# Optimization experiments

Measured on AMD Instinct MI355X. Metric: run time of the kernel, lower is better.

Reference implementation:

```python
import jax, jax.numpy as jnp
import numpy as np

L, D, H, DK, FF, R, N, B = 8, 256, 8, 32, 1024, 37, 1024, 1
EPS = 1e-6


def setup_inputs() -> dict:
    key = jax.random.key(0)
    ks = jax.random.split(key, 16)
    def w(i, shape, s=0.05):
        return jax.random.normal(ks[i], shape, jnp.float32) * s
    return {
        "x": jax.random.normal(ks[0], (B, N, D), jnp.float32),
        "relations": jax.random.randint(ks[1], (N, N), 0, R),
        "Wq": w(2, (L, D, D)), "bq": jnp.zeros((L, D), jnp.float32),
        "Wk": w(3, (L, D, D)), "bk": jnp.zeros((L, D), jnp.float32),
        "Wv": w(4, (L, D, D)), "bv": jnp.zeros((L, D), jnp.float32),
        "Wo": w(5, (L, D, D)), "bo": jnp.zeros((L, D), jnp.float32),
        "rel_k_emb": w(6, (L, R, DK)), "rel_v_emb": w(7, (L, R, DK)),
        "W1": w(8, (L, D, FF)), "b1": jnp.zeros((L, FF), jnp.float32),
        "W2": w(9, (L, FF, D)), "b2": jnp.zeros((L, D), jnp.float32),
        "ln1_g": jnp.ones((L, D), jnp.float32), "ln1_b": jnp.zeros((L, D), jnp.float32),
        "ln2_g": jnp.ones((L, D), jnp.float32), "ln2_b": jnp.zeros((L, D), jnp.float32),
        "lnf_g": jnp.ones((D,), jnp.float32), "lnf_b": jnp.zeros((D,), jnp.float32),
    }


def _layernorm(h, g, b):
    # Annotated-Transformer LayerNorm: g*(x-mu)/(std+eps)+b with unbiased std
    mu = h.mean(-1, keepdims=True)
    sd = jnp.sqrt(h.var(-1, keepdims=True, ddof=1))
    return g * (h - mu) / (sd + EPS) + b


def reference(x, relations, Wq, bq, Wk, bk, Wv, bv, Wo, bo,
              rel_k_emb, rel_v_emb, W1, b1, W2, b2,
              ln1_g, ln1_b, ln2_g, ln2_b, lnf_g, lnf_b):
    Bb, n, d = x.shape
    scale = 1.0 / jnp.sqrt(jnp.float32(DK))
    for l in range(L):
        # --- relation-aware self-attention sublayer (pre-norm residual) ---
        xn = _layernorm(x, ln1_g[l], ln1_b[l])
        q = (xn @ Wq[l] + bq[l]).reshape(Bb, n, H, DK).transpose(0, 2, 1, 3)
        k = (xn @ Wk[l] + bk[l]).reshape(Bb, n, H, DK).transpose(0, 2, 1, 3)
        v = (xn @ Wv[l] + bv[l]).reshape(Bb, n, H, DK).transpose(0, 2, 1, 3)
        rk = rel_k_emb[l][relations]  # [n, n, DK] irregular gather
        rv = rel_v_emb[l][relations]  # [n, n, DK]
        scores = (jnp.einsum('bhid,bhjd->bhij', q, k)
                  + jnp.einsum('bhid,ijd->bhij', q, rk)) * scale
        p = jax.nn.softmax(scores, axis=-1)
        o = (jnp.einsum('bhij,bhjd->bhid', p, v)
             + jnp.einsum('bhij,ijd->bhid', p, rv))
        o = o.transpose(0, 2, 1, 3).reshape(Bb, n, d) @ Wo[l] + bo[l]
        x = x + o
        # --- position-wise FFN sublayer (pre-norm residual) ---
        xn = _layernorm(x, ln2_g[l], ln2_b[l])
        x = x + (jax.nn.relu(xn @ W1[l] + b1[l]) @ W2[l] + b2[l])
    return _layernorm(x, lnf_g, lnf_b)
```

## Files before the change

kernel.cpp:

```cpp
#include <hip/hip_runtime.h>
#include <stdint.h>

#define L_ 8
#define D_ 256
#define H_ 8
#define DK_ 32
#define FF_ 1024
#define R_ 37
#define N_ 1024
#define AIB 32

#define SCL (0.17677669529663689f * 1.4426950408889634f)

typedef float f4v __attribute__((ext_vector_type(4)));
typedef short b8v __attribute__((ext_vector_type(8)));
typedef uint  u2v __attribute__((ext_vector_type(2)));

__device__ __forceinline__ ushort f2b(float f){
  union { float f; uint32_t u; } x; x.f = f;
  return (ushort)((x.u + 0x7FFFu + ((x.u >> 16) & 1u)) >> 16);
}
__device__ __forceinline__ float b2f(ushort u){
  union { uint32_t u; float f; } x; x.u = ((uint32_t)u) << 16;
  return x.f;
}
__device__ __forceinline__ uint pk2b(float lo, float hi){
  return (((uint)f2b(hi)) << 16) | (uint)f2b(lo);
}
__device__ __forceinline__ float ex2(float x){ return __builtin_amdgcn_exp2f(x); }

__device__ __forceinline__ void lds_fadd(float* p, float v){
  asm volatile("ds_add_f32 %0, %1" :: "v"((uint)(uintptr_t)p), "v"(v) : "memory");
}

__global__ __launch_bounds__(256)
void wcast_kernel(const float* __restrict__ src, ushort* __restrict__ dst, int K, int Nc){
  __shared__ float t[32][33];
  int l = blockIdx.z;
  long base = (long)l * K * Nc;
  int n0 = blockIdx.x * 32, k0 = blockIdx.y * 32;
  int tx = threadIdx.x, ty = threadIdx.y;
  #pragma unroll
  for (int r = 0; r < 32; r += 8)
    t[ty + r][tx] = src[base + (long)(k0 + ty + r) * Nc + n0 + tx];
  __syncthreads();
  #pragma unroll
  for (int r = 0; r < 32; r += 8)
    dst[base + (long)(n0 + ty + r) * K + k0 + tx] = f2b(t[tx][ty + r]);
}

__global__ __launch_bounds__(256)
void rel8_kernel(const int* __restrict__ rel, uint* __restrict__ rel8){
  long idx = (long)blockIdx.x * 256 + threadIdx.x;
  int4 v = ((const int4*)rel)[idx];
  rel8[idx] = (uint)(v.x & 255) | ((uint)(v.y & 255) << 8)
            | ((uint)(v.z & 255) << 16) | ((uint)(v.w & 255) << 24);
}

template<int OUTB>
__global__ __launch_bounds__(64)
void ln_kernel(const float* __restrict__ x, const float* __restrict__ g, const float* __restrict__ b,
               ushort* __restrict__ ob, float* __restrict__ of){
  int row = blockIdx.x, lane = threadIdx.x;
  float4 v = ((const float4*)(x + (long)row * D_))[lane];
  float s = v.x + v.y + v.z + v.w;
  float s2 = v.x*v.x + v.y*v.y + v.z*v.z + v.w*v.w;
  #pragma unroll
  for (int o = 32; o; o >>= 1){ s += __shfl_xor(s, o); s2 += __shfl_xor(s2, o); }
  float mu = s * (1.f / D_);
  float var = (s2 - D_ * mu * mu) * (1.f / (D_ - 1));
  var = fmaxf(var, 0.f);
  float inv = 1.f / (sqrtf(var) + 1e-6f);
  float4 gv = ((const float4*)g)[lane];
  float4 bv = ((const float4*)b)[lane];
  float o0 = gv.x * (v.x - mu) * inv + bv.x;
  float o1 = gv.y * (v.y - mu) * inv + bv.y;
  float o2 = gv.z * (v.z - mu) * inv + bv.z;
  float o3 = gv.w * (v.w - mu) * inv + bv.w;
  if (OUTB){
    ushort4 u; u.x = f2b(o0); u.y = f2b(o1); u.z = f2b(o2); u.w = f2b(o3);
    ((ushort4*)ob)[(long)row * 64 + lane] = u;
  } else {
    float4 o; o.x = o0; o.y = o1; o.z = o2; o.w = o3;
    ((float4*)of)[(long)row * 64 + lane] = o;
  }
}

template<int QKV, int RELU, int RESID, int OUTF, int OUTB>
__global__ __launch_bounds__(256)
void gemm_kernel(const ushort* __restrict__ A,
                 const ushort* __restrict__ W0, const ushort* __restrict__ W1p, const ushort* __restrict__ W2p,
                 const float* __restrict__ B0, const float* __restrict__ B1p, const float* __restrict__ B2p,
                 float* __restrict__ resid, float* __restrict__ outF, ushort* __restrict__ outB,
                 ushort* __restrict__ outB2,
                 int M, int Nc, int K){
  __shared__ ushort Al[64 * 48];
  __shared__ ushort Bl[64 * 48];
  int tid = threadIdx.x;
  int lane = tid & 63, w = tid >> 6;
  int wm = w >> 1, wn = w & 1;
  int bn0 = blockIdx.x * 64, bm0 = blockIdx.y * 64;
  const ushort* WT; const float* bias; int wn0;
  if (QKV){
    int which = bn0 >> 8;
    WT = which == 0 ? W0 : (which == 1 ? W1p : W2p);
    bias = which == 0 ? B0 : (which == 1 ? B1p : B2p);
    wn0 = bn0 & 255;
  } else { WT = W0; bias = B0; wn0 = bn0; }

  int r4 = tid >> 2, c8 = (tid & 3) * 8;
  const ushort* ag = A + (long)(bm0 + r4) * K + c8;
  const ushort* bg = WT + (long)(wn0 + r4) * K + c8;

  f4v acc[2][2];
  #pragma unroll
  for (int i = 0; i < 2; ++i)
    #pragma unroll
    for (int j = 0; j < 2; ++j)
      acc[i][j] = (f4v){0.f, 0.f, 0.f, 0.f};

  int l16 = lane & 15, lg = lane >> 4;
  int arow0 = (wm * 32 + l16) * 48 + lg * 8;
  int brow0 = (wn * 32 + l16) * 48 + lg * 8;

  for (int k0 = 0; k0 < K; k0 += 32){
    b8v a8 = *(const b8v*)(ag + k0);
    b8v b8 = *(const b8v*)(bg + k0);
    __syncthreads();
    *(b8v*)&Al[r4 * 48 + c8] = a8;
    *(b8v*)&Bl[r4 * 48 + c8] = b8;
    __syncthreads();
    b8v a0 = *(const b8v*)&Al[arow0];
    b8v a1 = *(const b8v*)&Al[arow0 + 16 * 48];
    b8v b0 = *(const b8v*)&Bl[brow0];
    b8v b1 = *(const b8v*)&Bl[brow0 + 16 * 48];
    acc[0][0] = __builtin_amdgcn_mfma_f32_16x16x32_bf16(a0, b0, acc[0][0], 0, 0, 0);
    acc[0][1] = __builtin_amdgcn_mfma_f32_16x16x32_bf16(a0, b1, acc[0][1], 0, 0, 0);
    acc[1][0] = __builtin_amdgcn_mfma_f32_16x16x32_bf16(a1, b0, acc[1][0], 0, 0, 0);
    acc[1][1] = __builtin_amdgcn_mfma_f32_16x16x32_bf16(a1, b1, acc[1][1], 0, 0, 0);
  }
  #pragma unroll
  for (int fi = 0; fi < 2; ++fi)
    #pragma unroll
    for (int fj = 0; fj < 2; ++fj){
      int row0 = bm0 + wm * 32 + fi * 16 + lg * 4;
      int col = bn0 + wn * 32 + fj * 16 + l16;
      float vv[4];
      #pragma unroll
      for (int j = 0; j < 4; ++j) vv[j] = acc[fi][fj][j] + bias[QKV ? (col & 255) : col];
      if (QKV){
        int which = col >> 8, hh = (col >> 5) & 7, dk = col & 31;
        if (which == 2){
          ushort4 pk; pk.x = f2b(vv[0]); pk.y = f2b(vv[1]); pk.z = f2b(vv[2]); pk.w = f2b(vv[3]);
          *(ushort4*)(outB2 + (long)hh * 32768 + (long)dk * 1024 + row0) = pk;
        } else {
          #pragma unroll
          for (int j = 0; j < 4; ++j)
            outB[(long)which * 262144 + (long)hh * 32768 + (long)(row0 + j) * 32 + dk] = f2b(vv[j]);
        }
      } else {
        #pragma unroll
        for (int j = 0; j < 4; ++j){
          float v = vv[j];
          if (RELU) v = fmaxf(v, 0.f);
          long idx = (long)(row0 + j) * Nc + col;
          if (RESID) v += resid[idx];
          if (OUTF) outF[idx] = v;
          if (OUTB) outB[idx] = f2b(v);
        }
      }
    }
}

__global__ __launch_bounds__(512)
void attn_kernel(const ushort* __restrict__ qb, const ushort* __restrict__ kb,
                 const ushort* __restrict__ vbt, const float* __restrict__ rke,
                 const float* __restrict__ rve,
                 const unsigned char* __restrict__ rel8, ushort* __restrict__ ob){
  __shared__ float q_l[AIB * 32];
  __shared__ float qr_l[AIB * 40];
  __shared__ float prb[4 * AIB * 40];
  __shared__ uint  p_l[8 * 16 * 20];
  __shared__ float part_l[4 * AIB * 34];
  __shared__ float wf_l[4 * AIB];
  __shared__ float lrow_l[AIB];

  int tid = threadIdx.x, lane = tid & 63, w = tid >> 6;
  int l16 = lane & 15, g = lane >> 4;
  int ib0 = blockIdx.x * AIB, h = blockIdx.y;
  int js = w >> 1, ig = w & 1;
  int ir = ig * 16 + l16;

  if (tid < 256){
    int row = tid >> 3, d4 = (tid & 7) * 4;
    ushort4 u = *(const ushort4*)(qb + (long)((h << 10) + ib0 + row) * 32 + d4);
    q_l[row * 32 + d4 + 0] = b2f(u.x);
    q_l[row * 32 + d4 + 1] = b2f(u.y);
    q_l[row * 32 + d4 + 2] = b2f(u.z);
    q_l[row * 32 + d4 + 3] = b2f(u.w);
  }
  for (int idx = tid; idx < 4 * AIB * 40; idx += 512) prb[idx] = 0.f;
  __syncthreads();

  for (int slot = tid; slot < AIB * 40; slot += 512){
    int row = slot / 40, r = slot - row * 40;
    if (r < R_){
      const float* qh = &q_l[row * 32];
      const float* e = rke + r * 32;
      float acc = 0.f;
      #pragma unroll
      for (int d = 0; d < 32; ++d) acc += qh[d] * e[d];
      qr_l[slot] = acc * SCL;
    }
  }
  __syncthreads();

  b8v qf = *(const b8v*)(qb + (long)((h << 10) + ib0 + ir) * 32 + g * 8);

  f4v oacc0 = (f4v){0.f,0.f,0.f,0.f}, oacc1 = (f4v){0.f,0.f,0.f,0.f};
  float m = -3.0e38f, lsum = 0.f;
  const float* qrr = &qr_l[ir * 40];
  float* prr = &prb[(js * AIB + ir) * 40];
  const unsigned char* relrow = rel8 + (long)(ib0 + ir) * N_ + js * 256;
  const ushort* kbh = kb + (long)(h << 10) * 32;
  const ushort* vth = vbt + (long)h * 32 * 1024;
  uint* pw = &p_l[w * 320 + l16 * 20];

  #pragma unroll
  for (int jt = 0; jt < 8; ++jt){
    int j0 = js * 256 + jt * 32;
    b8v kf0 = *(const b8v*)(kbh + (long)(j0 + l16) * 32 + g * 8);
    b8v kf1 = *(const b8v*)(kbh + (long)(j0 + 16 + l16) * 32 + g * 8);
    b8v vt0 = *(const b8v*)(vth + (long)l16 * 1024 + j0 + g * 8);
    b8v vt1 = *(const b8v*)(vth + (long)(16 + l16) * 1024 + j0 + g * 8);
    uint rr0 = *(const uint*)(relrow + jt * 32 + g * 4);
    uint rr1 = *(const uint*)(relrow + jt * 32 + 16 + g * 4);

    f4v z = (f4v){0.f,0.f,0.f,0.f};
    f4v s0 = __builtin_amdgcn_mfma_f32_16x16x32_bf16(kf0, qf, z, 0, 0, 0);
    f4v s1 = __builtin_amdgcn_mfma_f32_16x16x32_bf16(kf1, qf, z, 0, 0, 0);

    int rix[8];
    float sv[8];
    #pragma unroll
    for (int e = 0; e < 4; ++e){
      rix[e]     = (rr0 >> (8 * e)) & 255;
      rix[e + 4] = (rr1 >> (8 * e)) & 255;
      sv[e]     = s0[e] * SCL + qrr[rix[e]];
      sv[e + 4] = s1[e] * SCL + qrr[rix[e + 4]];
    }
    float tmax = sv[0];
    #pragma unroll
    for (int e = 1; e < 8; ++e) tmax = fmaxf(tmax, sv[e]);
    tmax = fmaxf(tmax, __shfl_xor(tmax, 16));
    tmax = fmaxf(tmax, __shfl_xor(tmax, 32));

    if (tmax - m > 12.f){
      float f = ex2(m - tmax);
      oacc0 *= f; oacc1 *= f; lsum *= f;
      #pragma unroll
      for (int b2 = 0; b2 < 10; ++b2){
        int bi = g * 10 + b2;
        if (bi < R_) prr[bi] *= f;
      }
      m = tmax;
    }
    float p[8], ps = 0.f;
    #pragma unroll
    for (int e = 0; e < 8; ++e){ p[e] = ex2(sv[e] - m); ps += p[e]; }
    ps += __shfl_xor(ps, 16);
    ps += __shfl_xor(ps, 32);
    lsum += ps;
    #pragma unroll
    for (int e = 0; e < 8; ++e) lds_fadd(&prr[rix[e]], p[e]);

    uint pk0 = pk2b(p[0], p[1]), pk1 = pk2b(p[2], p[3]);
    uint pk2 = pk2b(p[4], p[5]), pk3 = pk2b(p[6], p[7]);
    *(u2v*)&pw[g * 2]     = (u2v){pk0, pk1};
    *(u2v*)&pw[8 + g * 2] = (u2v){pk2, pk3};
    b8v pf = *(const b8v*)&pw[g * 4];
    oacc0 = __builtin_amdgcn_mfma_f32_16x16x32_bf16(vt0, pf, oacc0, 0, 0, 0);
    oacc1 = __builtin_amdgcn_mfma_f32_16x16x32_bf16(vt1, pf, oacc1, 0, 0, 0);
  }

  {
    float* pp = &part_l[(js * AIB + ir) * 34];
    #pragma unroll
    for (int e = 0; e < 4; ++e){
      pp[g * 4 + e] = oacc0[e];
      pp[16 + g * 4 + e] = oacc1[e];
    }
    if (g == 0){ pp[32] = m; pp[33] = lsum; }
  }
  __syncthreads();

  if (tid < AIB){
    int row = tid;
    float ms[4], ls[4];
    float mstar = -3.0e38f;
    #pragma unroll
    for (int s = 0; s < 4; ++s){
      ms[s] = part_l[(s * AIB + row) * 34 + 32];
      ls[s] = part_l[(s * AIB + row) * 34 + 33];
      mstar = fmaxf(mstar, ms[s]);
    }
    float lstar = 0.f;
    #pragma unroll
    for (int s = 0; s < 4; ++s){
      float wfv = ex2(ms[s] - mstar);
      wf_l[s * AIB + row] = wfv;
      lstar += ls[s] * wfv;
    }
    lrow_l[row] = lstar;
  }
  __syncthreads();

  for (int slot = tid; slot < AIB * 40; slot += 512){
    int row = slot / 40;
    float acc = 0.f;
    #pragma unroll
    for (int s = 0; s < 4; ++s) acc += prb[(s * AIB) * 40 + slot] * wf_l[s * AIB + row];
    prb[slot] = acc;
  }
  __syncthreads();

  for (int slot = tid; slot < AIB * 32; slot += 512){
    int row = slot >> 5, d = slot & 31;
    float o1 = 0.f;
    #pragma unroll
    for (int s = 0; s < 4; ++s) o1 += part_l[(s * AIB + row) * 34 + d] * wf_l[s * AIB + row];
    float o2 = 0.f;
    #pragma unroll
    for (int r = 0; r < R_; ++r) o2 += prb[row * 40 + r] * rve[r * 32 + d];
    float val = (o1 + o2) / lrow_l[row];
    ob[(long)(ib0 + row) * D_ + h * 32 + d] = f2b(val);
  }
}

extern "C" void kernel_launch(void* const* d_in, const int* in_sizes, int n_in,
                              void* d_out, int out_size, void* d_ws, size_t ws_size,
                              hipStream_t stream){
  const float* x    = (const float*)d_in[0];
  const int*   rel  = (const int*)d_in[1];
  const float* Wq   = (const float*)d_in[2];
  const float* bq   = (const float*)d_in[3];
  const float* Wk   = (const float*)d_in[4];
  const float* bk   = (const float*)d_in[5];
  const float* Wv   = (const float*)d_in[6];
  const float* bv   = (const float*)d_in[7];
  const float* Wo   = (const float*)d_in[8];
  const float* bo   = (const float*)d_in[9];
  const float* rke  = (const float*)d_in[10];
  const float* rve  = (const float*)d_in[11];
  const float* W1   = (const float*)d_in[12];
  const float* b1   = (const float*)d_in[13];
  const float* W2   = (const float*)d_in[14];
  const float* b2   = (const float*)d_in[15];
  const float* ln1g = (const float*)d_in[16];
  const float* ln1b = (const float*)d_in[17];
  const float* ln2g = (const float*)d_in[18];
  const float* ln2b = (const float*)d_in[19];
  const float* lnfg = (const float*)d_in[20];
  const float* lnfb = (const float*)d_in[21];

  char* wsb = (char*)d_ws;
  size_t off = 0;
  auto alloc = [&](size_t bytes){ void* p = wsb + off; off += (bytes + 255) & ~255ull; return p; };
  float*  xw   = (float*) alloc((size_t)N_ * D_ * 4);
  ushort* qkvb = (ushort*)alloc((size_t)3 * H_ * N_ * DK_ * 2);
  ushort* vbt  = (ushort*)alloc((size_t)H_ * DK_ * N_ * 2);
  ushort* xnb  = (ushort*)alloc((size_t)N_ * D_ * 2);
  ushort* obf  = (ushort*)alloc((size_t)N_ * D_ * 2);
  ushort* hidb = (ushort*)alloc((size_t)N_ * FF_ * 2);
  uint*   rel8 = (uint*)  alloc((size_t)N_ * N_);
  ushort* wqT  = (ushort*)alloc((size_t)L_ * D_ * D_ * 2);
  ushort* wkT  = (ushort*)alloc((size_t)L_ * D_ * D_ * 2);
  ushort* wvT  = (ushort*)alloc((size_t)L_ * D_ * D_ * 2);
  ushort* woT  = (ushort*)alloc((size_t)L_ * D_ * D_ * 2);
  ushort* w1T  = (ushort*)alloc((size_t)L_ * D_ * FF_ * 2);
  ushort* w2T  = (ushort*)alloc((size_t)L_ * D_ * FF_ * 2);
  (void)ws_size; (void)in_sizes; (void)n_in; (void)out_size;

  ushort* qb = qkvb;
  ushort* kb = qkvb + (size_t)H_ * N_ * DK_;

  dim3 tb(32, 8);
  wcast_kernel<<<dim3(D_/32,  D_/32,  L_), tb, 0, stream>>>(Wq, wqT, D_, D_);
  wcast_kernel<<<dim3(D_/32,  D_/32,  L_), tb, 0, stream>>>(Wk, wkT, D_, D_);
  wcast_kernel<<<dim3(D_/32,  D_/32,  L_), tb, 0, stream>>>(Wv, wvT, D_, D_);
  wcast_kernel<<<dim3(D_/32,  D_/32,  L_), tb, 0, stream>>>(Wo, woT, D_, D_);
  wcast_kernel<<<dim3(FF_/32, D_/32,  L_), tb, 0, stream>>>(W1, w1T, D_, FF_);
  wcast_kernel<<<dim3(D_/32,  FF_/32, L_), tb, 0, stream>>>(W2, w2T, FF_, D_);
  rel8_kernel<<<N_ * N_ / 1024, 256, 0, stream>>>(rel, rel8);

  hipMemcpyAsync(xw, x, (size_t)N_ * D_ * 4, hipMemcpyDeviceToDevice, stream);

  for (int l = 0; l < L_; ++l){
    ln_kernel<1><<<N_, 64, 0, stream>>>(xw, ln1g + l * D_, ln1b + l * D_, xnb, nullptr);
    gemm_kernel<1,0,0,0,1><<<dim3(768/64, N_/64), 256, 0, stream>>>(
        xnb, wqT + (size_t)l * D_ * D_, wkT + (size_t)l * D_ * D_, wvT + (size_t)l * D_ * D_,
        bq + l * D_, bk + l * D_, bv + l * D_,
        nullptr, nullptr, qkvb, vbt, N_, 768, D_);
    attn_kernel<<<dim3(N_/AIB, H_), 512, 0, stream>>>(
        qb, kb, vbt, rke + (size_t)l * R_ * DK_, rve + (size_t)l * R_ * DK_,
        (const unsigned char*)rel8, obf);
    gemm_kernel<0,0,1,1,0><<<dim3(D_/64, N_/64), 256, 0, stream>>>(
        obf, woT + (size_t)l * D_ * D_, nullptr, nullptr,
        bo + l * D_, nullptr, nullptr,
        xw, xw, nullptr, nullptr, N_, D_, D_);
    ln_kernel<1><<<N_, 64, 0, stream>>>(xw, ln2g + l * D_, ln2b + l * D_, xnb, nullptr);
    gemm_kernel<0,1,0,0,1><<<dim3(FF_/64, N_/64), 256, 0, stream>>>(
        xnb, w1T + (size_t)l * D_ * FF_, nullptr, nullptr,
        b1 + l * FF_, nullptr, nullptr,
        nullptr, nullptr, hidb, nullptr, N_, FF_, D_);
    gemm_kernel<0,0,1,1,0><<<dim3(D_/64, N_/64), 256, 0, stream>>>(
        hidb, w2T + (size_t)l * FF_ * D_, nullptr, nullptr,
        b2 + l * D_, nullptr, nullptr,
        xw, xw, nullptr, nullptr, N_, D_, FF_);
  }
  ln_kernel<0><<<N_, 64, 0, stream>>>(xw, lnfg, lnfb, nullptr, (float*)d_out);
}
```

Baseline: 784.9 us.

## Split attention key range across eight waves with 16-row query blocks and prefetch

```diff
diff --git a/kernel.cpp b/kernel.cpp
--- a/kernel.cpp
+++ b/kernel.cpp
@@ -8,7 +8,7 @@
 #define FF_ 1024
 #define R_ 37
 #define N_ 1024
-#define AIB 32
+#define AIB 16
 
 #define SCL (0.17677669529663689f * 1.4426950408889634f)
 
@@ -179,19 +179,19 @@
                  const unsigned char* __restrict__ rel8, ushort* __restrict__ ob){
   __shared__ float q_l[AIB * 32];
   __shared__ float qr_l[AIB * 40];
-  __shared__ float prb[4 * AIB * 40];
-  __shared__ uint  p_l[8 * 16 * 20];
-  __shared__ float part_l[4 * AIB * 34];
-  __shared__ float wf_l[4 * AIB];
+  __shared__ float prb[8 * AIB * 41];
+  __shared__ uint  p_l[8 * AIB * 20];
+  __shared__ float part_l[8 * AIB * 33];
+  __shared__ float wf_l[8 * AIB];
+  __shared__ float ls_l[8 * AIB];
   __shared__ float lrow_l[AIB];
 
   int tid = threadIdx.x, lane = tid & 63, w = tid >> 6;
   int l16 = lane & 15, g = lane >> 4;
   int ib0 = blockIdx.x * AIB, h = blockIdx.y;
-  int js = w >> 1, ig = w & 1;
-  int ir = ig * 16 + l16;
-
-  if (tid < 256){
+  int ir = l16;
+
+  if (tid < 128){
     int row = tid >> 3, d4 = (tid & 7) * 4;
     ushort4 u = *(const ushort4*)(qb + (long)((h << 10) + ib0 + row) * 32 + d4);
     q_l[row * 32 + d4 + 0] = b2f(u.x);
@@ -199,7 +199,7 @@
     q_l[row * 32 + d4 + 2] = b2f(u.z);
     q_l[row * 32 + d4 + 3] = b2f(u.w);
   }
-  for (int idx = tid; idx < 4 * AIB * 40; idx += 512) prb[idx] = 0.f;
+  for (int idx = tid; idx < 8 * AIB * 41; idx += 512) prb[idx] = 0.f;
   __syncthreads();
 
   for (int slot = tid; slot < AIB * 40; slot += 512){
@@ -218,120 +218,144 @@
   b8v qf = *(const b8v*)(qb + (long)((h << 10) + ib0 + ir) * 32 + g * 8);
 
   f4v oacc0 = (f4v){0.f,0.f,0.f,0.f}, oacc1 = (f4v){0.f,0.f,0.f,0.f};
-  float m = -3.0e38f, lsum = 0.f;
+  float m = -3.0e38f;
   const float* qrr = &qr_l[ir * 40];
-  float* prr = &prb[(js * AIB + ir) * 40];
-  const unsigned char* relrow = rel8 + (long)(ib0 + ir) * N_ + js * 256;
+  float* prr = &prb[(w * AIB + ir) * 41];
+  const unsigned char* relrow = rel8 + (long)(ib0 + ir) * N_ + w * 128;
   const ushort* kbh = kb + (long)(h << 10) * 32;
   const ushort* vth = vbt + (long)h * 32 * 1024;
-  uint* pw = &p_l[w * 320 + l16 * 20];
-
-  #pragma unroll
-  for (int jt = 0; jt < 8; ++jt){
-    int j0 = js * 256 + jt * 32;
-    b8v kf0 = *(const b8v*)(kbh + (long)(j0 + l16) * 32 + g * 8);
-    b8v kf1 = *(const b8v*)(kbh + (long)(j0 + 16 + l16) * 32 + g * 8);
-    b8v vt0 = *(const b8v*)(vth + (long)l16 * 1024 + j0 + g * 8);
-    b8v vt1 = *(const b8v*)(vth + (long)(16 + l16) * 1024 + j0 + g * 8);
-    uint rr0 = *(const uint*)(relrow + jt * 32 + g * 4);
-    uint rr1 = *(const uint*)(relrow + jt * 32 + 16 + g * 4);
+  uint* pw = &p_l[(w * AIB + l16) * 20];
+
+  uint raw[8];
+  #pragma unroll
+  for (int t = 0; t < 4; ++t){
+    raw[t * 2]     = *(const uint*)(relrow + t * 32 + g * 4);
+    raw[t * 2 + 1] = *(const uint*)(relrow + t * 32 + 16 + g * 4);
+  }
+  float qv[32];
+  #pragma unroll
+  for (int t = 0; t < 4; ++t)
+    #pragma unroll
+    for (int e = 0; e < 4; ++e){
+      qv[t * 8 + e]     = qrr[(raw[t * 2]     >> (8 * e)) & 255];
+      qv[t * 8 + 4 + e] = qrr[(raw[t * 2 + 1] >> (8 * e)) & 255];
+    }
+
+  int jb = w * 128;
+  b8v kf0c = *(const b8v*)(kbh + (long)(jb + l16) * 32 + g * 8);
+  b8v kf1c = *(const b8v*)(kbh + (long)(jb + 16 + l16) * 32 + g * 8);
+  b8v vt0c = *(const b8v*)(vth + (long)l16 * 1024 + jb + g * 8);
+  b8v vt1c = *(const b8v*)(vth + (long)(16 + l16) * 1024 + jb + g * 8);
+
+  #pragma unroll
+  for (int t = 0; t < 4; ++t){
+    int j1 = jb + ((t + 1) & 3) * 32;
+    b8v kf0n = *(const b8v*)(kbh + (long)(j1 + l16) * 32 + g * 8);
+    b8v kf1n = *(const b8v*)(kbh + (long)(j1 + 16 + l16) * 32 + g * 8);
+    b8v vt0n = *(const b8v*)(vth + (long)l16 * 1024 + j1 + g * 8);
+    b8v vt1n = *(const b8v*)(vth + (long)(16 + l16) * 1024 + j1 + g * 8);
 
     f4v z = (f4v){0.f,0.f,0.f,0.f};
-    f4v s0 = __builtin_amdgcn_mfma_f32_16x16x32_bf16(kf0, qf, z, 0, 0, 0);
-    f4v s1 = __builtin_amdgcn_mfma_f32_16x16x32_bf16(kf1, qf, z, 0, 0, 0);
-
-    int rix[8];
+    f4v s0 = __builtin_amdgcn_mfma_f32_16x16x32_bf16(kf0c, qf, z, 0, 0, 0);
+    f4v s1 = __builtin_amdgcn_mfma_f32_16x16x32_bf16(kf1c, qf, z, 0, 0, 0);
+
     float sv[8];
     #pragma unroll
     for (int e = 0; e < 4; ++e){
-      rix[e]     = (rr0 >> (8 * e)) & 255;
-      rix[e + 4] = (rr1 >> (8 * e)) & 255;
-      sv[e]     = s0[e] * SCL + qrr[rix[e]];
-      sv[e + 4] = s1[e] * SCL + qrr[rix[e + 4]];
-    }
-    float tmax = sv[0];
-    #pragma unroll
-    for (int e = 1; e < 8; ++e) tmax = fmaxf(tmax, sv[e]);
-    tmax = fmaxf(tmax, __shfl_xor(tmax, 16));
-    tmax = fmaxf(tmax, __shfl_xor(tmax, 32));
-
-    if (tmax - m > 12.f){
-      float f = ex2(m - tmax);
-      oacc0 *= f; oacc1 *= f; lsum *= f;
-      #pragma unroll
-      for (int b2 = 0; b2 < 10; ++b2){
-        int bi = g * 10 + b2;
-        if (bi < R_) prr[bi] *= f;
+      sv[e]     = s0[e] * SCL + qv[t * 8 + e];
+      sv[e + 4] = s1[e] * SCL + qv[t * 8 + 4 + e];
+    }
+    float lmax = sv[0];
+    #pragma unroll
+    for (int e = 1; e < 8; ++e) lmax = fmaxf(lmax, sv[e]);
+
+    if (__any(lmax - m > 12.f)){
+      float tmax = fmaxf(lmax, __shfl_xor(lmax, 16));
+      tmax = fmaxf(tmax, __shfl_xor(tmax, 32));
+      if (tmax > m){
+        float f = ex2(m - tmax);
+        oacc0 *= f; oacc1 *= f;
+        #pragma unroll
+        for (int b2 = 0; b2 < 10; ++b2){
+          int bi = g * 10 + b2;
+          if (bi < R_) prr[bi] *= f;
+        }
+        m = tmax;
       }
-      m = tmax;
-    }
-    float p[8], ps = 0.f;
-    #pragma unroll
-    for (int e = 0; e < 8; ++e){ p[e] = ex2(sv[e] - m); ps += p[e]; }
-    ps += __shfl_xor(ps, 16);
-    ps += __shfl_xor(ps, 32);
-    lsum += ps;
-    #pragma unroll
-    for (int e = 0; e < 8; ++e) lds_fadd(&prr[rix[e]], p[e]);
+    }
+    float p[8];
+    #pragma unroll
+    for (int e = 0; e < 8; ++e) p[e] = ex2(sv[e] - m);
+    #pragma unroll
+    for (int e = 0; e < 4; ++e){
+      lds_fadd(&prr[(raw[t * 2]     >> (8 * e)) & 255], p[e]);
+      lds_fadd(&prr[(raw[t * 2 + 1] >> (8 * e)) & 255], p[e + 4]);
+    }
 
     uint pk0 = pk2b(p[0], p[1]), pk1 = pk2b(p[2], p[3]);
     uint pk2 = pk2b(p[4], p[5]), pk3 = pk2b(p[6], p[7]);
     *(u2v*)&pw[g * 2]     = (u2v){pk0, pk1};
     *(u2v*)&pw[8 + g * 2] = (u2v){pk2, pk3};
     b8v pf = *(const b8v*)&pw[g * 4];
-    oacc0 = __builtin_amdgcn_mfma_f32_16x16x32_bf16(vt0, pf, oacc0, 0, 0, 0);
-    oacc1 = __builtin_amdgcn_mfma_f32_16x16x32_bf16(vt1, pf, oacc1, 0, 0, 0);
+    oacc0 = __builtin_amdgcn_mfma_f32_16x16x32_bf16(vt0c, pf, oacc0, 0, 0, 0);
+    oacc1 = __builtin_amdgcn_mfma_f32_16x16x32_bf16(vt1c, pf, oacc1, 0, 0, 0);
+
+    kf0c = kf0n; kf1c = kf1n; vt0c = vt0n; vt1c = vt1n;
   }
 
   {
-    float* pp = &part_l[(js * AIB + ir) * 34];
+    float* pp = &part_l[(w * AIB + ir) * 33];
     #pragma unroll
     for (int e = 0; e < 4; ++e){
       pp[g * 4 + e] = oacc0[e];
       pp[16 + g * 4 + e] = oacc1[e];
     }
-    if (g == 0){ pp[32] = m; pp[33] = lsum; }
+    if (g == 0) pp[32] = m;
+  }
+  __syncthreads();
+
+  for (int slot = tid; slot < 8 * AIB; slot += 512){
+    const float* pb = &prb[slot * 41];
+    float acc = 0.f;
+    #pragma unroll
+    for (int r = 0; r < R_; ++r) acc += pb[r];
+    ls_l[slot] = acc;
   }
   __syncthreads();
 
   if (tid < AIB){
     int row = tid;
-    float ms[4], ls[4];
     float mstar = -3.0e38f;
     #pragma unroll
-    for (int s = 0; s < 4; ++s){
-      ms[s] = part_l[(s * AIB + row) * 34 + 32];
-      ls[s] = part_l[(s * AIB + row) * 34 + 33];
-      mstar = fmaxf(mstar, ms[s]);
-    }
+    for (int s = 0; s < 8; ++s) mstar = fmaxf(mstar, part_l[(s * AIB + row) * 33 + 32]);
     float lstar = 0.f;
     #pragma unroll
-    for (int s = 0; s < 4; ++s){
-      float wfv = ex2(ms[s] - mstar);
+    for (int s = 0; s < 8; ++s){
+      float wfv = ex2(part_l[(s * AIB + row) * 33 + 32] - mstar);
       wf_l[s * AIB + row] = wfv;
-      lstar += ls[s] * wfv;
+      lstar += ls_l[s * AIB + row] * wfv;
     }
     lrow_l[row] = lstar;
   }
   __syncthreads();
 
-  for (int slot = tid; slot < AIB * 40; slot += 512){
-    int row = slot / 40;
+  for (int slot = tid; slot < AIB * 41; slot += 512){
+    int row = slot / 41;
     float acc = 0.f;
     #pragma unroll
-    for (int s = 0; s < 4; ++s) acc += prb[(s * AIB) * 40 + slot] * wf_l[s * AIB + row];
+    for (int s = 0; s < 8; ++s) acc += prb[s * AIB * 41 + slot] * wf_l[s * AIB + row];
     prb[slot] = acc;
   }
   __syncthreads();
 
-  for (int slot = tid; slot < AIB * 32; slot += 512){
-    int row = slot >> 5, d = slot & 31;
+  {
+    int row = tid >> 5, d = tid & 31;
     float o1 = 0.f;
     #pragma unroll
-    for (int s = 0; s < 4; ++s) o1 += part_l[(s * AIB + row) * 34 + d] * wf_l[s * AIB + row];
+    for (int s = 0; s < 8; ++s) o1 += part_l[(s * AIB + row) * 33 + d] * wf_l[s * AIB + row];
     float o2 = 0.f;
     #pragma unroll
-    for (int r = 0; r < R_; ++r) o2 += prb[row * 40 + r] * rve[r * 32 + d];
+    for (int r = 0; r < R_; ++r) o2 += prb[row * 41 + r] * rve[r * 32 + d];
     float val = (o1 + o2) / lrow_l[row];
     ob[(long)(ib0 + row) * D_ + h * 32 + d] = f2b(val);
   }
```

Measured after the change: 787.4 us. Within noise of the previous version (+0.3%).
